# Performance work log

Hardware: AMD Instinct MI355X
Metric: run time of the kernel (lower is better)

Reference implementation:

```python
import jax, jax.numpy as jnp
import numpy as np

IN_F, OUT_F, GROUP = 4096, 11008, 128

# NF4 codebook (normalized-float-4 levels), matches NF4_LEVELS in the source
NF4_LEVELS = jnp.array([
    -1.0, -0.6961928009986877, -0.5250730514526367, -0.39491748809814453,
    -0.28444138169288635, -0.18477343022823334, -0.09105003625154495, 0.0,
    0.07958029955625534, 0.16093020141124725, 0.24611230194568634,
    0.33791524171829224, 0.44070982933044434, 0.5626170039176941,
    0.7229568362236023, 1.0], dtype=jnp.float32)


def setup_inputs() -> dict:
    key = jax.random.key(0)
    k0, k1, k2, k3 = jax.random.split(key, 4)
    x = jax.random.normal(k0, (32, 1, IN_F), dtype=jnp.float32)
    # one int32 per packed byte; low nibble = even element code, high nibble = odd
    packed = jax.random.randint(k1, (OUT_F * IN_F // 2,), 0, 256, dtype=jnp.int32)
    # per-group absmax scales (positive)
    scales = jax.random.uniform(k2, (OUT_F * IN_F // GROUP,), dtype=jnp.float32) * 0.02 + 1e-4
    bias_param = jax.random.normal(k3, (OUT_F,), dtype=jnp.float32)
    return {"x": x, "packed": packed, "scales": scales, "bias_param": bias_param}


def dequant_nf4(packed, scales):
    # unpack two 4-bit codes per byte; interleave as quantized[0::2]=low, [1::2]=high
    low = packed & 15
    high = (packed >> 4) & 15
    codes = jnp.stack([low, high], axis=-1).reshape(-1)          # [OUT_F*IN_F]
    vals = NF4_LEVELS[codes]                                      # codebook lookup
    w = (vals.reshape(-1, GROUP) * scales[:, None]).reshape(OUT_F, IN_F)
    return w


def reference(x, packed, scales, bias_param):
    W = dequant_nf4(packed, scales)                               # [OUT_F, IN_F]
    # y = x @ W^T + b  (F.linear semantics)
    return jnp.einsum('bsi,oi->bso', x, W) + bias_param
```

## Files before the change

kernel.cpp:

```cpp
#include <hip/hip_runtime.h>
#include <hip/hip_bf16.h>

#define IN_F   4096
#define OUT_F  11008
#define BATCH  32
#define NTILE  16
#define GRID_N (OUT_F / NTILE)

typedef __attribute__((ext_vector_type(8))) short  bf16x8;
typedef __attribute__((ext_vector_type(4))) float  f32x4;
typedef __attribute__((ext_vector_type(4))) int    i32x4;
typedef __attribute__((ext_vector_type(4))) float  float4v;

static __device__ __constant__ float NF4_LEVELS[16] = {
    -1.0f, -0.6961928009986877f, -0.5250730514526367f, -0.39491748809814453f,
    -0.28444138169288635f, -0.18477343022823334f, -0.09105003625154495f, 0.0f,
    0.07958029955625534f, 0.16093020141124725f, 0.24611230194568634f,
    0.33791524171829224f, 0.44070982933044434f, 0.5626170039176941f,
    0.7229568362236023f, 1.0f};

__global__ void prelude_kernel(const float* __restrict__ x,
                               unsigned short* __restrict__ frag) {
    int T  = blockIdx.x * 256 + threadIdx.x;
    int st = T >> 13;
    int kb = (T >> 6) & 127;
    int l  = T & 63;
    int row = st * 16 + (l & 15);
    int k0  = kb * 32 + (l >> 4) * 8;
    const float* src = x + (size_t)row * IN_F + k0;
    unsigned w[4];
    #pragma unroll
    for (int e = 0; e < 4; ++e) {
        unsigned lo = __builtin_bit_cast(unsigned short, __float2bfloat16(src[2 * e]));
        unsigned hi = __builtin_bit_cast(unsigned short, __float2bfloat16(src[2 * e + 1]));
        w[e] = lo | (hi << 16);
    }
    i32x4 v = { (int)w[0], (int)w[1], (int)w[2], (int)w[3] };
    *reinterpret_cast<i32x4*>(frag + ((size_t)st * 8192 + kb * 64 + l) * 8) = v;
}

__global__ __launch_bounds__(256, 3) void nf4_gemm_kernel(
        const int* __restrict__ packed,
        const float* __restrict__ scales,
        const float* __restrict__ bias,
        const unsigned short* __restrict__ frag,
        float* __restrict__ out)
{
    __shared__ unsigned lds[9216];

    const int tid  = threadIdx.x;
    const int wave = tid >> 6;
    const int lane = tid & 63;
    const int col  = lane & 15;
    const int g    = lane >> 4;

    const int n0 = blockIdx.x * NTILE;

    #pragma unroll
    for (int q = 0; q < 4; ++q) {
        int e = q * 64 + lane;
        unsigned lo = __builtin_bit_cast(unsigned short, __float2bfloat16(NF4_LEVELS[e & 15]));
        unsigned hi = __builtin_bit_cast(unsigned short, __float2bfloat16(NF4_LEVELS[(e >> 4) & 15]));
        lds[wave * 256 + e] = lo | (hi << 16);
    }

    float scw[8];
    {
        const float* sp = scales + (size_t)(n0 + col) * 32 + wave * 8;
        float4v sv0 = *reinterpret_cast<const float4v*>(sp);
        float4v sv1 = *reinterpret_cast<const float4v*>(sp + 4);
        scw[0]=sv0.x; scw[1]=sv0.y; scw[2]=sv0.z; scw[3]=sv0.w;
        scw[4]=sv1.x; scw[5]=sv1.y; scw[6]=sv1.z; scw[7]=sv1.w;
    }

    const int dperm = (lane & 0x30) | ((lane & 3) << 2) | ((lane >> 2) & 3);

    #define PLOAD(u, r0, sr)                                                   \
        _Pragma("unroll")                                                      \
        for (int ii = 0; ii < 8; ++ii) {                                       \
            sr[ii] = *reinterpret_cast<const i32x4*>(                          \
                packed + (size_t)(n0 + (r0) + ii) * (IN_F / 2)                 \
                       + wave * 512 + (u) * 256 + lane * 4);                   \
        }

    #define PWRITE(u, r0, sr)                                                  \
        _Pragma("unroll")                                                      \
        for (int ii = 0; ii < 8; ++ii) {                                       \
            int row = (r0) + ii;                                               \
            unsigned v = ((unsigned)(sr[ii][0] & 255))                         \
                       | ((unsigned)(sr[ii][1] & 255) << 8)                    \
                       | ((unsigned)(sr[ii][2] & 255) << 16)                   \
                       | ((unsigned)(sr[ii][3] & 255) << 24);                  \
            lds[1024 + (wave * 2 + (u)) * 1024                                 \
                + ((row * 64 + dperm) ^ ((row & 7) << 2))] = v;                \
        }

    f32x4 acc0 = (f32x4){0.f,0.f,0.f,0.f};
    f32x4 acc1 = (f32x4){0.f,0.f,0.f,0.f};

    const unsigned short* f0 = frag;
    const unsigned short* f1 = frag + 65536;

    #define COMPUTE_GRP(u, grp)                                                \
    {                                                                          \
        i32x4 cd = *reinterpret_cast<const i32x4*>(                            \
            &lds[1024 + (wave * 2 + (u)) * 1024                                \
                 + ((col * 64 + (grp) * 16 + g * 4) ^ ((col & 7) << 2))]);     \
        bf16x8 A0[4], A1[4];                                                   \
        _Pragma("unroll")                                                      \
        for (int t = 0; t < 4; ++t) {                                          \
            int kb = wave * 32 + (u) * 16 + (grp) * 4 + t;                     \
            A0[t] = *reinterpret_cast<const bf16x8*>(f0 + ((size_t)kb * 64 + lane) * 8); \
            A1[t] = *reinterpret_cast<const bf16x8*>(f1 + ((size_t)kb * 64 + lane) * 8); \
        }                                                                      \
        f32x4 t0 = (f32x4){0.f,0.f,0.f,0.f};                                   \
        f32x4 t1 = (f32x4){0.f,0.f,0.f,0.f};                                   \
        _Pragma("unroll")                                                      \
        for (int t = 0; t < 4; ++t) {                                          \
            unsigned code = (unsigned)cd[t];                                   \
            i32x4 bu;                                                          \
            bu[0] = (int)lds[wave * 256 + (code & 255u)];                      \
            bu[1] = (int)lds[wave * 256 + ((code >> 8) & 255u)];               \
            bu[2] = (int)lds[wave * 256 + ((code >> 16) & 255u)];              \
            bu[3] = (int)lds[wave * 256 + (code >> 24)];                       \
            bf16x8 bf = __builtin_bit_cast(bf16x8, bu);                        \
            t0 = __builtin_amdgcn_mfma_f32_16x16x32_bf16(A0[t], bf, t0, 0, 0, 0); \
            t1 = __builtin_amdgcn_mfma_f32_16x16x32_bf16(A1[t], bf, t1, 0, 0, 0); \
        }                                                                      \
        const float sc = scw[(u) * 4 + (grp)];                                 \
        _Pragma("unroll")                                                      \
        for (int j = 0; j < 4; ++j) {                                          \
            acc0[j] = fmaf(sc, t0[j], acc0[j]);                                \
            acc1[j] = fmaf(sc, t1[j], acc1[j]);                                \
        }                                                                      \
    }

    i32x4 sa[8], sb[8];
    PLOAD(0, 0, sa)
    PLOAD(0, 8, sb)
    PWRITE(0, 0, sa)
    PWRITE(0, 8, sb)

    COMPUTE_GRP(0, 0)
    PLOAD(1, 0, sa)
    COMPUTE_GRP(0, 1)
    PLOAD(1, 8, sb)
    COMPUTE_GRP(0, 2)
    COMPUTE_GRP(0, 3)

    PWRITE(1, 0, sa)
    PWRITE(1, 8, sb)
    COMPUTE_GRP(1, 0)
    COMPUTE_GRP(1, 1)
    COMPUTE_GRP(1, 2)
    COMPUTE_GRP(1, 3)

    float* red = (float*)&lds[1024 + wave * 2048];
    #pragma unroll
    for (int j = 0; j < 4; ++j) {
        red[(0 * 4 + j) * 64 + g * 16 + col] = acc0[j];
        red[(1 * 4 + j) * 64 + g * 16 + col] = acc1[j];
    }
    __syncthreads();

    #pragma unroll
    for (int p = 0; p < 2; ++p) {
        int idx = p * 256 + tid;
        int b   = idx >> 4;
        int c   = idx & 15;
        int h   = b >> 4;
        int r   = b & 15;
        int j   = r & 3;
        int g2  = r >> 2;
        int slot = (h * 4 + j) * 64 + g2 * 16 + c;
        const float* rbase = (const float*)&lds[1024];
        float s = rbase[slot] + rbase[2048 / 4 * 4 + slot]
                + rbase[4096 + slot] + rbase[6144 + slot];
        out[(size_t)b * OUT_F + n0 + c] = s + bias[n0 + c];
    }
}

extern "C" void kernel_launch(void* const* d_in, const int* in_sizes, int n_in,
                              void* d_out, int out_size, void* d_ws, size_t ws_size,
                              hipStream_t stream) {
    const float* x      = (const float*)d_in[0];
    const int*   packed = (const int*)d_in[1];
    const float* scales = (const float*)d_in[2];
    const float* bias   = (const float*)d_in[3];
    float* out = (float*)d_out;

    unsigned short* frag = (unsigned short*)d_ws;

    prelude_kernel<<<64, 256, 0, stream>>>(x, frag);
    nf4_gemm_kernel<<<GRID_N, 256, 0, stream>>>(packed, scales, bias, frag, out);
}
```

Baseline: 28.02 us.

## Split waves over batch halves and K halves with 4-stage code pipeline

```diff
diff --git a/kernel.cpp b/kernel.cpp
--- a/kernel.cpp
+++ b/kernel.cpp
@@ -53,6 +53,8 @@
     const int lane = tid & 63;
     const int col  = lane & 15;
     const int g    = lane >> 4;
+    const int bh   = wave >> 1;
+    const int kh   = wave & 1;
 
     const int n0 = blockIdx.x * NTILE;
 
@@ -64,105 +66,86 @@
         lds[wave * 256 + e] = lo | (hi << 16);
     }
 
-    float scw[8];
-    {
-        const float* sp = scales + (size_t)(n0 + col) * 32 + wave * 8;
-        float4v sv0 = *reinterpret_cast<const float4v*>(sp);
-        float4v sv1 = *reinterpret_cast<const float4v*>(sp + 4);
-        scw[0]=sv0.x; scw[1]=sv0.y; scw[2]=sv0.z; scw[3]=sv0.w;
-        scw[4]=sv1.x; scw[5]=sv1.y; scw[6]=sv1.z; scw[7]=sv1.w;
-    }
+    const int dperm = (lane & 0x30) | ((lane & 3) << 2) | ((lane >> 2) & 3);
+    unsigned* cbase = &lds[1024 + wave * 2048];
 
-    const int dperm = (lane & 0x30) | ((lane & 3) << 2) | ((lane >> 2) & 3);
-
-    #define PLOAD(u, r0, sr)                                                   \
+    #define SL8(u, r0, sr)                                                     \
         _Pragma("unroll")                                                      \
         for (int ii = 0; ii < 8; ++ii) {                                       \
             sr[ii] = *reinterpret_cast<const i32x4*>(                          \
                 packed + (size_t)(n0 + (r0) + ii) * (IN_F / 2)                 \
-                       + wave * 512 + (u) * 256 + lane * 4);                   \
+                       + kh * 1024 + (u) * 256 + lane * 4);                    \
         }
 
-    #define PWRITE(u, r0, sr)                                                  \
+    #define SW8(u, r0, sr)                                                     \
         _Pragma("unroll")                                                      \
         for (int ii = 0; ii < 8; ++ii) {                                       \
-            int row = (r0) + ii;                                               \
+            int rl = (r0) + ii;                                                \
             unsigned v = ((unsigned)(sr[ii][0] & 255))                         \
                        | ((unsigned)(sr[ii][1] & 255) << 8)                    \
                        | ((unsigned)(sr[ii][2] & 255) << 16)                   \
                        | ((unsigned)(sr[ii][3] & 255) << 24);                  \
-            lds[1024 + (wave * 2 + (u)) * 1024                                 \
-                + ((row * 64 + dperm) ^ ((row & 7) << 2))] = v;                \
+            cbase[((u) & 1) * 1024 + ((rl * 64 + dperm) ^ ((rl & 7) << 2))] = v; \
         }
 
-    f32x4 acc0 = (f32x4){0.f,0.f,0.f,0.f};
-    f32x4 acc1 = (f32x4){0.f,0.f,0.f,0.f};
+    f32x4 acc = (f32x4){0.f, 0.f, 0.f, 0.f};
+    const unsigned short* fb = frag + bh * 65536;
 
-    const unsigned short* f0 = frag;
-    const unsigned short* f1 = frag + 65536;
-
-    #define COMPUTE_GRP(u, grp)                                                \
+    #define COMPUTE(u)                                                         \
     {                                                                          \
-        i32x4 cd = *reinterpret_cast<const i32x4*>(                            \
-            &lds[1024 + (wave * 2 + (u)) * 1024                                \
-                 + ((col * 64 + (grp) * 16 + g * 4) ^ ((col & 7) << 2))]);     \
-        bf16x8 A0[4], A1[4];                                                   \
+        float4v scv = *reinterpret_cast<const float4v*>(                       \
+            scales + (size_t)(n0 + col) * 32 + kh * 16 + (u) * 4);             \
+        const float sca[4] = { scv.x, scv.y, scv.z, scv.w };                   \
         _Pragma("unroll")                                                      \
-        for (int t = 0; t < 4; ++t) {                                          \
-            int kb = wave * 32 + (u) * 16 + (grp) * 4 + t;                     \
-            A0[t] = *reinterpret_cast<const bf16x8*>(f0 + ((size_t)kb * 64 + lane) * 8); \
-            A1[t] = *reinterpret_cast<const bf16x8*>(f1 + ((size_t)kb * 64 + lane) * 8); \
-        }                                                                      \
-        f32x4 t0 = (f32x4){0.f,0.f,0.f,0.f};                                   \
-        f32x4 t1 = (f32x4){0.f,0.f,0.f,0.f};                                   \
-        _Pragma("unroll")                                                      \
-        for (int t = 0; t < 4; ++t) {                                          \
-            unsigned code = (unsigned)cd[t];                                   \
-            i32x4 bu;                                                          \
-            bu[0] = (int)lds[wave * 256 + (code & 255u)];                      \
-            bu[1] = (int)lds[wave * 256 + ((code >> 8) & 255u)];               \
-            bu[2] = (int)lds[wave * 256 + ((code >> 16) & 255u)];              \
-            bu[3] = (int)lds[wave * 256 + (code >> 24)];                       \
-            bf16x8 bf = __builtin_bit_cast(bf16x8, bu);                        \
-            t0 = __builtin_amdgcn_mfma_f32_16x16x32_bf16(A0[t], bf, t0, 0, 0, 0); \
-            t1 = __builtin_amdgcn_mfma_f32_16x16x32_bf16(A1[t], bf, t1, 0, 0, 0); \
-        }                                                                      \
-        const float sc = scw[(u) * 4 + (grp)];                                 \
-        _Pragma("unroll")                                                      \
-        for (int j = 0; j < 4; ++j) {                                          \
-            acc0[j] = fmaf(sc, t0[j], acc0[j]);                                \
-            acc1[j] = fmaf(sc, t1[j], acc1[j]);                                \
+        for (int grp = 0; grp < 4; ++grp) {                                    \
+            bf16x8 A[4];                                                       \
+            _Pragma("unroll")                                                  \
+            for (int t = 0; t < 4; ++t) {                                      \
+                int kb = kh * 64 + (u) * 16 + grp * 4 + t;                     \
+                A[t] = *reinterpret_cast<const bf16x8*>(                       \
+                    fb + ((size_t)kb * 64 + lane) * 8);                        \
+            }                                                                  \
+            i32x4 cd = *reinterpret_cast<const i32x4*>(                        \
+                &cbase[((u) & 1) * 1024 +                                      \
+                       ((col * 64 + grp * 16 + g * 4) ^ ((col & 7) << 2))]);   \
+            f32x4 tt = (f32x4){0.f, 0.f, 0.f, 0.f};                            \
+            _Pragma("unroll")                                                  \
+            for (int t = 0; t < 4; ++t) {                                      \
+                unsigned code = (unsigned)cd[t];                               \
+                i32x4 bu;                                                      \
+                bu[0] = (int)lds[wave * 256 + (code & 255u)];                  \
+                bu[1] = (int)lds[wave * 256 + ((code >> 8) & 255u)];           \
+                bu[2] = (int)lds[wave * 256 + ((code >> 16) & 255u)];          \
+                bu[3] = (int)lds[wave * 256 + (code >> 24)];                   \
+                tt = __builtin_amdgcn_mfma_f32_16x16x32_bf16(                  \
+                    A[t], __builtin_bit_cast(bf16x8, bu), tt, 0, 0, 0);        \
+            }                                                                  \
+            _Pragma("unroll")                                                  \
+            for (int j = 0; j < 4; ++j)                                        \
+                acc[j] = fmaf(sca[grp], tt[j], acc[j]);                        \
         }                                                                      \
     }
 
-    i32x4 sa[8], sb[8];
-    PLOAD(0, 0, sa)
-    PLOAD(0, 8, sb)
-    PWRITE(0, 0, sa)
-    PWRITE(0, 8, sb)
+    i32x4 s0[8], s1[8];
+    SL8(0, 0, s0) SL8(0, 8, s1) SW8(0, 0, s0) SW8(0, 8, s1)
+    SL8(1, 0, s0) SL8(1, 8, s1)
+    COMPUTE(0)
+    SW8(1, 0, s0) SW8(1, 8, s1)
+    SL8(2, 0, s0) SL8(2, 8, s1)
+    COMPUTE(1)
+    SW8(2, 0, s0) SW8(2, 8, s1)
+    SL8(3, 0, s0) SL8(3, 8, s1)
+    COMPUTE(2)
+    SW8(3, 0, s0) SW8(3, 8, s1)
+    COMPUTE(3)
 
-    COMPUTE_GRP(0, 0)
-    PLOAD(1, 0, sa)
-    COMPUTE_GRP(0, 1)
-    PLOAD(1, 8, sb)
-    COMPUTE_GRP(0, 2)
-    COMPUTE_GRP(0, 3)
-
-    PWRITE(1, 0, sa)
-    PWRITE(1, 8, sb)
-    COMPUTE_GRP(1, 0)
-    COMPUTE_GRP(1, 1)
-    COMPUTE_GRP(1, 2)
-    COMPUTE_GRP(1, 3)
-
-    float* red = (float*)&lds[1024 + wave * 2048];
+    float* red = (float*)cbase;
     #pragma unroll
-    for (int j = 0; j < 4; ++j) {
-        red[(0 * 4 + j) * 64 + g * 16 + col] = acc0[j];
-        red[(1 * 4 + j) * 64 + g * 16 + col] = acc1[j];
-    }
+    for (int j = 0; j < 4; ++j)
+        red[j * 64 + g * 16 + col] = acc[j];
     __syncthreads();
 
+    const float* rbase = (const float*)&lds[1024];
     #pragma unroll
     for (int p = 0; p < 2; ++p) {
         int idx = p * 256 + tid;
@@ -172,10 +155,9 @@
         int r   = b & 15;
         int j   = r & 3;
         int g2  = r >> 2;
-        int slot = (h * 4 + j) * 64 + g2 * 16 + c;
-        const float* rbase = (const float*)&lds[1024];
-        float s = rbase[slot] + rbase[2048 / 4 * 4 + slot]
-                + rbase[4096 + slot] + rbase[6144 + slot];
+        int slot = j * 64 + g2 * 16 + c;
+        float s = rbase[(h * 2 + 0) * 2048 + slot]
+                + rbase[(h * 2 + 1) * 2048 + slot];
         out[(size_t)b * OUT_F + n0 + c] = s + bias[n0 + c];
     }
 }
```

New measurement: 30.75 us. 1.1x slower.

## Replicate NF4 byte table across LDS banks and reuse single code buffer per wave

Applied to the files above, without the earlier changes.

```diff
diff --git a/kernel.cpp b/kernel.cpp
--- a/kernel.cpp
+++ b/kernel.cpp
@@ -46,22 +46,25 @@
         const unsigned short* __restrict__ frag,
         float* __restrict__ out)
 {
-    __shared__ unsigned lds[9216];
+    __shared__ unsigned tab32[8192];
+    __shared__ unsigned codes[4096];
 
     const int tid  = threadIdx.x;
     const int wave = tid >> 6;
     const int lane = tid & 63;
     const int col  = lane & 15;
     const int g    = lane >> 4;
+    const int lr   = lane & 31;
 
     const int n0 = blockIdx.x * NTILE;
 
     #pragma unroll
-    for (int q = 0; q < 4; ++q) {
-        int e = q * 64 + lane;
-        unsigned lo = __builtin_bit_cast(unsigned short, __float2bfloat16(NF4_LEVELS[e & 15]));
-        unsigned hi = __builtin_bit_cast(unsigned short, __float2bfloat16(NF4_LEVELS[(e >> 4) & 15]));
-        lds[wave * 256 + e] = lo | (hi << 16);
+    for (int q = 0; q < 32; ++q) {
+        int i = q * 256 + tid;
+        int c = i >> 5;
+        unsigned lo = __builtin_bit_cast(unsigned short, __float2bfloat16(NF4_LEVELS[c & 15]));
+        unsigned hi = __builtin_bit_cast(unsigned short, __float2bfloat16(NF4_LEVELS[(c >> 4) & 15]));
+        tab32[i] = lo | (hi << 16);
     }
 
     float scw[8];
@@ -73,7 +76,10 @@
         scw[4]=sv1.x; scw[5]=sv1.y; scw[6]=sv1.z; scw[7]=sv1.w;
     }
 
+    __syncthreads();
+
     const int dperm = (lane & 0x30) | ((lane & 3) << 2) | ((lane >> 2) & 3);
+    unsigned* cbuf = &codes[wave * 1024];
 
     #define PLOAD(u, r0, sr)                                                   \
         _Pragma("unroll")                                                      \
@@ -83,7 +89,7 @@
                        + wave * 512 + (u) * 256 + lane * 4);                   \
         }
 
-    #define PWRITE(u, r0, sr)                                                  \
+    #define PWRITE(r0, sr)                                                     \
         _Pragma("unroll")                                                      \
         for (int ii = 0; ii < 8; ++ii) {                                       \
             int row = (r0) + ii;                                               \
@@ -91,8 +97,7 @@
                        | ((unsigned)(sr[ii][1] & 255) << 8)                    \
                        | ((unsigned)(sr[ii][2] & 255) << 16)                   \
                        | ((unsigned)(sr[ii][3] & 255) << 24);                  \
-            lds[1024 + (wave * 2 + (u)) * 1024                                 \
-                + ((row * 64 + dperm) ^ ((row & 7) << 2))] = v;                \
+            cbuf[(row * 64 + dperm) ^ ((row & 7) << 2)] = v;                   \
         }
 
     f32x4 acc0 = (f32x4){0.f,0.f,0.f,0.f};
@@ -104,8 +109,7 @@
     #define COMPUTE_GRP(u, grp)                                                \
     {                                                                          \
         i32x4 cd = *reinterpret_cast<const i32x4*>(                            \
-            &lds[1024 + (wave * 2 + (u)) * 1024                                \
-                 + ((col * 64 + (grp) * 16 + g * 4) ^ ((col & 7) << 2))]);     \
+            &cbuf[(col * 64 + (grp) * 16 + g * 4) ^ ((col & 7) << 2)]);        \
         bf16x8 A0[4], A1[4];                                                   \
         _Pragma("unroll")                                                      \
         for (int t = 0; t < 4; ++t) {                                          \
@@ -119,10 +123,10 @@
         for (int t = 0; t < 4; ++t) {                                          \
             unsigned code = (unsigned)cd[t];                                   \
             i32x4 bu;                                                          \
-            bu[0] = (int)lds[wave * 256 + (code & 255u)];                      \
-            bu[1] = (int)lds[wave * 256 + ((code >> 8) & 255u)];               \
-            bu[2] = (int)lds[wave * 256 + ((code >> 16) & 255u)];              \
-            bu[3] = (int)lds[wave * 256 + (code >> 24)];                       \
+            bu[0] = (int)tab32[((code & 255u) << 5) | lr];                     \
+            bu[1] = (int)tab32[(((code >> 8) & 255u) << 5) | lr];              \
+            bu[2] = (int)tab32[(((code >> 16) & 255u) << 5) | lr];             \
+            bu[3] = (int)tab32[((code >> 24) << 5) | lr];                      \
             bf16x8 bf = __builtin_bit_cast(bf16x8, bu);                        \
             t0 = __builtin_amdgcn_mfma_f32_16x16x32_bf16(A0[t], bf, t0, 0, 0, 0); \
             t1 = __builtin_amdgcn_mfma_f32_16x16x32_bf16(A1[t], bf, t1, 0, 0, 0); \
@@ -136,26 +140,24 @@
     }
 
     i32x4 sa[8], sb[8];
-    PLOAD(0, 0, sa)
-    PLOAD(0, 8, sb)
-    PWRITE(0, 0, sa)
-    PWRITE(0, 8, sb)
+    PLOAD(0, 0, sa) PLOAD(0, 8, sb)
+    PWRITE(0, sa)  PWRITE(8, sb)
+
+    PLOAD(1, 0, sa) PLOAD(1, 8, sb)
 
     COMPUTE_GRP(0, 0)
-    PLOAD(1, 0, sa)
     COMPUTE_GRP(0, 1)
-    PLOAD(1, 8, sb)
     COMPUTE_GRP(0, 2)
     COMPUTE_GRP(0, 3)
 
-    PWRITE(1, 0, sa)
-    PWRITE(1, 8, sb)
+    PWRITE(0, sa)  PWRITE(8, sb)
+
     COMPUTE_GRP(1, 0)
     COMPUTE_GRP(1, 1)
     COMPUTE_GRP(1, 2)
     COMPUTE_GRP(1, 3)
 
-    float* red = (float*)&lds[1024 + wave * 2048];
+    float* red = (float*)cbuf;
     #pragma unroll
     for (int j = 0; j < 4; ++j) {
         red[(0 * 4 + j) * 64 + g * 16 + col] = acc0[j];
@@ -163,6 +165,7 @@
     }
     __syncthreads();
 
+    const float* rbase = (const float*)codes;
     #pragma unroll
     for (int p = 0; p < 2; ++p) {
         int idx = p * 256 + tid;
@@ -173,9 +176,8 @@
         int j   = r & 3;
         int g2  = r >> 2;
         int slot = (h * 4 + j) * 64 + g2 * 16 + c;
-        const float* rbase = (const float*)&lds[1024];
-        float s = rbase[slot] + rbase[2048 / 4 * 4 + slot]
-                + rbase[4096 + slot] + rbase[6144 + slot];
+        float s = rbase[slot] + rbase[1024 + slot]
+                + rbase[2048 + slot] + rbase[3072 + slot];
         out[(size_t)b * OUT_F + n0 + c] = s + bias[n0 + c];
     }
 }
```

Measured after the change: 28.49 us. No clear change (+1.7%).
